# Optimization experiments

Hardware: AMD Instinct MI355X
Metric: run time of the kernel (lower is better)

Reference implementation:

```python
import jax, jax.numpy as jnp
import numpy as np
import math

B, S, HID = 1, 4096, 2048
H, KVH, D = 32, 8, 64
N_REP = H // KVH  # 4


def _rope(x, cos, sin):
    # x: [B, h, S, D]; cos/sin: [S, D//2]
    x2 = x.reshape(*x.shape[:-1], D // 2, 2)
    x0, x1 = x2[..., 0], x2[..., 1]
    c = cos[None, None, :, :]
    s = sin[None, None, :, :]
    # complex multiply (x0 + i x1) * (c + i s)
    o0 = x0 * c - x1 * s
    o1 = x0 * s + x1 * c
    return jnp.stack([o0, o1], axis=-1).reshape(x.shape)


def setup_inputs() -> dict:
    key = jax.random.key(0)
    ks = jax.random.split(key, 6)
    hidden_states = jax.random.normal(ks[0], (B, S, 2 * HID), dtype=jnp.float32)
    scale = 0.02
    wq = jax.random.normal(ks[1], (H * D, 2 * HID), dtype=jnp.float32) * scale
    wk = jax.random.normal(ks[2], (KVH * D, 2 * HID), dtype=jnp.float32) * scale
    wv = jax.random.normal(ks[3], (KVH * D, 2 * HID), dtype=jnp.float32) * scale
    wo = jax.random.normal(ks[4], (HID, H * D), dtype=jnp.float32) * scale
    # standard RoPE frequencies (theta=10000), shape [S, D//2]
    inv_freq = 1.0 / (10000.0 ** (np.arange(0, D, 2, dtype=np.float32) / D))
    angles = np.arange(S, dtype=np.float32)[:, None] * inv_freq[None, :]
    freqs_cos = jnp.asarray(np.cos(angles), dtype=jnp.float32)
    freqs_sin = jnp.asarray(np.sin(angles), dtype=jnp.float32)
    return {"hidden_states": hidden_states, "wq": wq, "wk": wk, "wv": wv,
            "wo": wo, "freqs_cos": freqs_cos, "freqs_sin": freqs_sin}


def reference(hidden_states, wq, wk, wv, wo, freqs_cos, freqs_sin):
    bsz, q_len, _ = hidden_states.shape
    q = (hidden_states @ wq.T).reshape(bsz, q_len, H, D).transpose(0, 2, 1, 3)   # [B,H,S,D]
    k = (hidden_states @ wk.T).reshape(bsz, q_len, KVH, D).transpose(0, 2, 1, 3)  # [B,KVH,S,D]
    v = (hidden_states @ wv.T).reshape(bsz, q_len, KVH, D).transpose(0, 2, 1, 3)
    q = _rope(q, freqs_cos, freqs_sin)
    k = _rope(k, freqs_cos, freqs_sin)
    # GQA repeat_kv
    k = jnp.repeat(k, N_REP, axis=1)  # [B,H,S,D]
    v = jnp.repeat(v, N_REP, axis=1)
    scores = jnp.einsum('bhqd,bhkd->bhqk', q, k) / math.sqrt(D)  # [B,H,S,S]
    weights = jax.nn.softmax(scores.astype(jnp.float32), axis=-1).astype(q.dtype)
    attn = jnp.einsum('bhqk,bhkd->bhqd', weights, v)  # [B,H,S,D]
    attn = attn.transpose(0, 2, 1, 3).reshape(bsz, q_len, H * D)
    return attn @ wo.T  # [B,S,HID]
```

## Files before the change

### kernel.cpp

```cpp
#include <hip/hip_runtime.h>
#include <hip/hip_bf16.h>

typedef __attribute__((ext_vector_type(4))) float f32x4;
typedef __attribute__((ext_vector_type(8))) __bf16 bf16x8;
typedef __attribute__((ext_vector_type(8))) short short8;
typedef __attribute__((ext_vector_type(4))) short short4v;
typedef __attribute__((ext_vector_type(2))) unsigned int uint2v;

#define SEQ 4096
#define NQKV 3072

static __device__ __forceinline__ unsigned short f2bf(float x) {
  unsigned int u = __float_as_uint(x);
  u += 0x7fffu + ((u >> 16) & 1u);
  return (unsigned short)(u >> 16);
}
static __device__ __forceinline__ float bf2f(unsigned short b) {
  return __uint_as_float(((unsigned int)b) << 16);
}
static __device__ __forceinline__ unsigned int cvtpk_bf16(float lo, float hi) {
  unsigned int r;
  asm("v_cvt_pk_bf16_f32 %0, %1, %2" : "=v"(r) : "v"(lo), "v"(hi));
  return r;
}
static __device__ __forceinline__ float exp2_fast(float x) {
  float r;
  asm("v_exp_f32 %0, %1" : "=v"(r) : "v"(x));
  return r;
}

__global__ void cvt_f32_bf16(const float* __restrict__ src,
                             unsigned short* __restrict__ dst, int n4) {
  int i = blockIdx.x * blockDim.x + threadIdx.x;
  if (i >= n4) return;
  f32x4 v = ((const f32x4*)src)[i];
  short4v o;
#pragma unroll
  for (int j = 0; j < 4; ++j) o[j] = (short)f2bf(v[j]);
  ((short4v*)dst)[i] = o;
}

template <bool OUT_F32>
__global__ __launch_bounds__(256) void gemm_bt(const unsigned short* __restrict__ A,
                                               const unsigned short* __restrict__ Bt,
                                               void* __restrict__ Cp,
                                               int M, int N, int K) {
  __shared__ unsigned short As[128 * 32];
  __shared__ unsigned short Bs[128 * 32];
  const int l = threadIdx.x & 63;
  const int wid = threadIdx.x >> 6;
  const int wr = wid >> 1, wc = wid & 1;
  const int m0 = blockIdx.y * 128, n0 = blockIdx.x * 128;
  const int lr = l & 15, lg = l >> 4;
  const int srow = l >> 2;
  const int scol = (l & 3) * 8;

  f32x4 acc[4][4];
#pragma unroll
  for (int i = 0; i < 4; ++i)
#pragma unroll
    for (int j = 0; j < 4; ++j) acc[i][j] = (f32x4){0.f, 0.f, 0.f, 0.f};

  for (int kt = 0; kt < K; kt += 32) {
#pragma unroll
    for (int i = 0; i < 2; ++i) {
      const int s = wid * 2 + i;
      const unsigned short* ga = A + (size_t)(m0 + s * 16 + srow) * K + kt + scol;
      __builtin_amdgcn_global_load_lds((const __attribute__((address_space(1))) void*)ga,
                                       (__attribute__((address_space(3))) void*)(As + s * 512),
                                       16, 0, 0);
      const unsigned short* gb = Bt + (size_t)(n0 + s * 16 + srow) * K + kt + scol;
      __builtin_amdgcn_global_load_lds((const __attribute__((address_space(1))) void*)gb,
                                       (__attribute__((address_space(3))) void*)(Bs + s * 512),
                                       16, 0, 0);
    }
    asm volatile("s_waitcnt vmcnt(0)" ::: "memory");
    __syncthreads();

    bf16x8 af[4], bfr[4];
#pragma unroll
    for (int i = 0; i < 4; ++i)
      af[i] = *(const bf16x8*)(As + (wr * 64 + i * 16 + lr) * 32 + lg * 8);
#pragma unroll
    for (int j = 0; j < 4; ++j)
      bfr[j] = *(const bf16x8*)(Bs + (wc * 64 + j * 16 + lr) * 32 + lg * 8);
#pragma unroll
    for (int i = 0; i < 4; ++i)
#pragma unroll
      for (int j = 0; j < 4; ++j)
        acc[i][j] = __builtin_amdgcn_mfma_f32_16x16x32_bf16(af[i], bfr[j], acc[i][j], 0, 0, 0);
    __syncthreads();
  }

  const int row0 = m0 + wr * 64, col0 = n0 + wc * 64;
#pragma unroll
  for (int i = 0; i < 4; ++i) {
#pragma unroll
    for (int j = 0; j < 4; ++j) {
      const int col = col0 + j * 16 + lr;
#pragma unroll
      for (int r = 0; r < 4; ++r) {
        const int row = row0 + i * 16 + lg * 4 + r;
        if (OUT_F32)
          ((float*)Cp)[(size_t)row * N + col] = acc[i][j][r];
        else
          ((unsigned short*)Cp)[(size_t)row * N + col] = f2bf(acc[i][j][r]);
      }
    }
  }
}

__global__ void rope_scale(unsigned short* __restrict__ qkv,
                           const float* __restrict__ fc,
                           const float* __restrict__ fs) {
  int idx = blockIdx.x * blockDim.x + threadIdx.x;
  int s = idx / 1280;
  int p = idx - s * 1280;
  bool isQ = (p < 1024);
  int col = isQ ? (p * 2) : (2048 + (p - 1024) * 2);
  int fi = (col >> 1) & 31;
  float c = fc[s * 32 + fi];
  float sn = fs[s * 32 + fi];
  unsigned short* ptr = qkv + (size_t)s * NQKV + col;
  float x0 = bf2f(ptr[0]);
  float x1 = bf2f(ptr[1]);
  float o0 = x0 * c - x1 * sn;
  float o1 = x0 * sn + x1 * c;
  float scl = isQ ? 0.1803368801111204f : 1.0f;
  ptr[0] = f2bf(o0 * scl);
  ptr[1] = f2bf(o1 * scl);
}

__global__ void v_transpose(const unsigned short* __restrict__ qkv,
                            unsigned short* __restrict__ Vt) {
  __shared__ unsigned short tile[64][72];
  const int kvh = blockIdx.x;
  const int st = blockIdx.y * 64;
  const int t = threadIdx.x;
  const int sl = t >> 2, d0 = (t & 3) * 16;
  const unsigned short* src = qkv + (size_t)(st + sl) * NQKV + 2560 + kvh * 64 + d0;
  *(bf16x8*)&tile[sl][d0] = *(const bf16x8*)src;
  *(bf16x8*)&tile[sl][d0 + 8] = *(const bf16x8*)(src + 8);
  __syncthreads();
  const int dl = t >> 2, s0 = (t & 3) * 16;
  unsigned short* dst = Vt + ((size_t)kvh * 64 + dl) * 4096 + st + s0;
#pragma unroll
  for (int j2 = 0; j2 < 2; ++j2) {
    short8 v;
#pragma unroll
    for (int j = 0; j < 8; ++j) v[j] = (short)tile[s0 + j2 * 8 + j][dl];
    *(short8*)(dst + j2 * 8) = v;
  }
}

__global__ __launch_bounds__(256, 4) void attn_fwd(const unsigned short* __restrict__ qkv,
                                                   const unsigned short* __restrict__ Vt,
                                                   unsigned short* __restrict__ attn) {
  __shared__ unsigned short Ks[2][4096];
  __shared__ unsigned short Vs[2][4096];
  __shared__ unsigned short Plds[4][1024];

  const int t = threadIdx.x;
  const int l = t & 63;
  const int w = t >> 6;
  const int lr = l & 15, lg = l >> 4;
  const int h = blockIdx.x;
  const int kvh = h >> 2;
  const int qbase = blockIdx.y * 128 + w * 32;

  const int chunk0 = w * 2;
  const int srow = l >> 3;
  const int scol = (l & 7) * 16;
  const int sorig = scol ^ ((srow & 7) << 4);
  const char* ksrc0 = (const char*)(qkv + 2048 + kvh * 64) +
                      (size_t)(chunk0 * 8 + srow) * (NQKV * 2) + sorig;
  const char* ksrc1 = ksrc0 + 8 * (NQKV * 2);
  const char* vsrc0 = (const char*)(Vt + (size_t)kvh * 64 * 4096) +
                      (size_t)(chunk0 * 8 + srow) * 8192 + sorig;
  const char* vsrc1 = vsrc0 + 8 * 8192;

  const int x = (lr & 7) << 4;
  const int x6 = x & 64, x45 = x & 48;
  const int offA = lr * 128 + x6 + ((lg * 16) ^ x45);
  const int offB = lr * 128 + (64 ^ x6) + ((lg * 16) ^ x45);

  const int pswz = ((lr & 7) << 4) ^ (w << 5);
  char* PldsB = (char*)Plds + w * 2048 + lr * 128;

  bf16x8 qf[2][2];
#pragma unroll
  for (int qi = 0; qi < 2; ++qi) {
    const unsigned short* qr = qkv + (size_t)(qbase + qi * 16 + lr) * NQKV + h * 64;
    qf[qi][0] = *(const bf16x8*)(qr + lg * 8);
    qf[qi][1] = *(const bf16x8*)(qr + 32 + lg * 8);
  }

  f32x4 ls4[2];
  f32x4 o[2][4];
#pragma unroll
  for (int qi = 0; qi < 2; ++qi) {
    ls4[qi] = (f32x4){0.f, 0.f, 0.f, 0.f};
#pragma unroll
    for (int c4 = 0; c4 < 4; ++c4) o[qi][c4] = (f32x4){0.f, 0.f, 0.f, 0.f};
  }

  auto stage = [&](int buf, int tile) {
    const size_t kadv = (size_t)tile * 64 * (NQKV * 2);
    const size_t vadv = (size_t)tile * 128;
    __builtin_amdgcn_global_load_lds(
        (const __attribute__((address_space(1))) void*)(ksrc0 + kadv),
        (__attribute__((address_space(3))) void*)&Ks[buf][chunk0 * 512], 16, 0, 0);
    __builtin_amdgcn_global_load_lds(
        (const __attribute__((address_space(1))) void*)(ksrc1 + kadv),
        (__attribute__((address_space(3))) void*)&Ks[buf][(chunk0 + 1) * 512], 16, 0, 0);
    __builtin_amdgcn_global_load_lds(
        (const __attribute__((address_space(1))) void*)(vsrc0 + vadv),
        (__attribute__((address_space(3))) void*)&Vs[buf][chunk0 * 512], 16, 0, 0);
    __builtin_amdgcn_global_load_lds(
        (const __attribute__((address_space(1))) void*)(vsrc1 + vadv),
        (__attribute__((address_space(3))) void*)&Vs[buf][(chunk0 + 1) * 512], 16, 0, 0);
  };

  stage(0, 0);
  asm volatile("s_waitcnt vmcnt(0)" ::: "memory");
  __syncthreads();

  const int NT = SEQ / 64;
  for (int tt = 0; tt < NT; ++tt) {
    const int buf = tt & 1;
    if (tt + 1 < NT) stage(buf ^ 1, tt + 1);

    const char* Ksb = (const char*)Ks[buf];
    const char* Vsb = (const char*)Vs[buf];

    f32x4 sc[2][4];
    __builtin_amdgcn_s_setprio(1);
#pragma unroll
    for (int sI = 0; sI < 4; ++sI) {
      bf16x8 kf0 = *(const bf16x8*)(Ksb + offA + sI * 2048);
      bf16x8 kf1 = *(const bf16x8*)(Ksb + offB + sI * 2048);
#pragma unroll
      for (int qi = 0; qi < 2; ++qi) {
        f32x4 c = (f32x4){0.f, 0.f, 0.f, 0.f};
        c = __builtin_amdgcn_mfma_f32_16x16x32_bf16(kf0, qf[qi][0], c, 0, 0, 0);
        c = __builtin_amdgcn_mfma_f32_16x16x32_bf16(kf1, qf[qi][1], c, 0, 0, 0);
        sc[qi][sI] = c;
      }
    }
    __builtin_amdgcn_s_setprio(0);

    bf16x8 pa[2][2];
#pragma unroll
    for (int qi = 0; qi < 2; ++qi) {
      float p[4][4];
#pragma unroll
      for (int sI = 0; sI < 4; ++sI)
#pragma unroll
        for (int r = 0; r < 4; ++r) p[sI][r] = exp2_fast(sc[qi][sI][r]);
#pragma unroll
      for (int sI = 0; sI < 4; ++sI)
#pragma unroll
        for (int r = 0; r < 4; ++r) ls4[qi][r] += p[sI][r];
#pragma unroll
      for (int sI = 0; sI < 4; ++sI) {
        uint2v pk;
        pk[0] = cvtpk_bf16(p[sI][0], p[sI][1]);
        pk[1] = cvtpk_bf16(p[sI][2], p[sI][3]);
        *(uint2v*)(PldsB + ((32 * sI + 8 * lg) ^ pswz)) = pk;
      }
      pa[qi][0] = *(const bf16x8*)(PldsB + ((16 * lg) ^ pswz));
      pa[qi][1] = *(const bf16x8*)(PldsB + ((64 + 16 * lg) ^ pswz));
    }

    __builtin_amdgcn_s_setprio(1);
#pragma unroll
    for (int c4 = 0; c4 < 4; ++c4) {
      bf16x8 v0 = *(const bf16x8*)(Vsb + offA + c4 * 2048);
      bf16x8 v1 = *(const bf16x8*)(Vsb + offB + c4 * 2048);
#pragma unroll
      for (int qi = 0; qi < 2; ++qi) {
        o[qi][c4] = __builtin_amdgcn_mfma_f32_16x16x32_bf16(pa[qi][0], v0, o[qi][c4], 0, 0, 0);
        o[qi][c4] = __builtin_amdgcn_mfma_f32_16x16x32_bf16(pa[qi][1], v1, o[qi][c4], 0, 0, 0);
      }
    }
    __builtin_amdgcn_s_setprio(0);

    asm volatile("s_waitcnt vmcnt(0)" ::: "memory");
    __syncthreads();
  }

#pragma unroll
  for (int qi = 0; qi < 2; ++qi) {
    float lsum = ls4[qi][0] + ls4[qi][1] + ls4[qi][2] + ls4[qi][3];
    lsum += __shfl_xor(lsum, 16, 64);
    lsum += __shfl_xor(lsum, 32, 64);
    float inv = 1.f / lsum;
    float invO[4];
#pragma unroll
    for (int r = 0; r < 4; ++r) invO[r] = __shfl(inv, 4 * lg + r, 64);
#pragma unroll
    for (int c4 = 0; c4 < 4; ++c4)
#pragma unroll
      for (int r = 0; r < 4; ++r) {
        attn[(size_t)(qbase + qi * 16 + 4 * lg + r) * 2048 + h * 64 + c4 * 16 + lr] =
            f2bf(o[qi][c4][r] * invO[r]);
      }
  }
}

extern "C" void kernel_launch(void* const* d_in, const int* in_sizes, int n_in,
                              void* d_out, int out_size, void* d_ws, size_t ws_size,
                              hipStream_t stream) {
  const float* hs = (const float*)d_in[0];
  const float* wq = (const float*)d_in[1];
  const float* wk = (const float*)d_in[2];
  const float* wv = (const float*)d_in[3];
  const float* wo = (const float*)d_in[4];
  const float* fc = (const float*)d_in[5];
  const float* fs = (const float*)d_in[6];
  float* out = (float*)d_out;

  char* ws = (char*)d_ws;
  unsigned short* Xb    = (unsigned short*)(ws);
  unsigned short* Wqkv  = (unsigned short*)(ws + (size_t)(32 << 20));
  unsigned short* Wob   = (unsigned short*)(ws + (size_t)(56 << 20));
  unsigned short* QKV   = (unsigned short*)(ws + (size_t)(64 << 20));
  unsigned short* attnb = Xb;
  unsigned short* Vtb   = (unsigned short*)(ws + (size_t)(16 << 20));

  cvt_f32_bf16<<<16384, 256, 0, stream>>>(hs, Xb, 4194304);
  cvt_f32_bf16<<<8192, 256, 0, stream>>>(wq, Wqkv, 2097152);
  cvt_f32_bf16<<<2048, 256, 0, stream>>>(wk, Wqkv + 8388608, 524288);
  cvt_f32_bf16<<<2048, 256, 0, stream>>>(wv, Wqkv + 10485760, 524288);
  cvt_f32_bf16<<<4096, 256, 0, stream>>>(wo, Wob, 1048576);

  gemm_bt<false><<<dim3(24, 32), 256, 0, stream>>>(Xb, Wqkv, QKV, 4096, 3072, 4096);

  v_transpose<<<dim3(8, 64), 256, 0, stream>>>(QKV, Vtb);
  rope_scale<<<20480, 256, 0, stream>>>(QKV, fc, fs);

  attn_fwd<<<dim3(32, 32), 256, 0, stream>>>(QKV, Vtb, attnb);

  gemm_bt<true><<<dim3(16, 32), 256, 0, stream>>>(attnb, Wob, out, 4096, 2048, 2048);
}
```

Before: 393.7 us.

## Replace GEMMs with 256-row tiles, triple-buffered LDS pipeline and swizzled loads

Both projection GEMMs are replaced by a 512-thread kernel that computes 256xBN tiles (BN=192 for QKV, 128 for the output projection). It uses three LDS buffers with prefetch two k-steps ahead, partial vmcnt waits and a single barrier per step, instead of a full drain plus two barriers each iteration. An XOR swizzle on the LDS layout reduces bank conflicts, and setprio raises wave priority around the MFMA block. The larger tiles raise MFMA work per LDS byte, at the cost of higher register and LDS pressure and fewer blocks (256 per GEMM) to fill the GPU.

```diff
diff --git a/kernel.cpp b/kernel.cpp
--- a/kernel.cpp
+++ b/kernel.cpp
@@ -40,63 +40,111 @@
   ((short4v*)dst)[i] = o;
 }
 
-template <bool OUT_F32>
-__global__ __launch_bounds__(256) void gemm_bt(const unsigned short* __restrict__ A,
-                                               const unsigned short* __restrict__ Bt,
-                                               void* __restrict__ Cp,
-                                               int M, int N, int K) {
-  __shared__ unsigned short As[128 * 32];
-  __shared__ unsigned short Bs[128 * 32];
-  const int l = threadIdx.x & 63;
-  const int wid = threadIdx.x >> 6;
-  const int wr = wid >> 1, wc = wid & 1;
-  const int m0 = blockIdx.y * 128, n0 = blockIdx.x * 128;
+template <int BN, bool OUT_F32>
+__global__ __launch_bounds__(512, 2) void gemm256(const unsigned short* __restrict__ A,
+                                                  const unsigned short* __restrict__ Bt,
+                                                  void* __restrict__ Cp,
+                                                  int M, int N, int K) {
+  constexpr int NJ = BN / 64;
+  constexpr int TC = 16 + BN / 16;
+  constexpr int SPW = (TC + 7) / 8;
+  constexpr int DUP = 8 * SPW - TC;
+
+  __shared__ unsigned short AbL[3][8192];
+  __shared__ unsigned short BbL[3][BN * 32];
+
+  const int t512 = threadIdx.x;
+  const int l = t512 & 63;
+  const int wid = t512 >> 6;
+  const int wm = wid >> 2, wn = wid & 3;
   const int lr = l & 15, lg = l >> 4;
-  const int srow = l >> 2;
-  const int scol = (l & 3) * 8;
-
-  f32x4 acc[4][4];
-#pragma unroll
-  for (int i = 0; i < 4; ++i)
-#pragma unroll
-    for (int j = 0; j < 4; ++j) acc[i][j] = (f32x4){0.f, 0.f, 0.f, 0.f};
-
-  for (int kt = 0; kt < K; kt += 32) {
-#pragma unroll
-    for (int i = 0; i < 2; ++i) {
-      const int s = wid * 2 + i;
-      const unsigned short* ga = A + (size_t)(m0 + s * 16 + srow) * K + kt + scol;
-      __builtin_amdgcn_global_load_lds((const __attribute__((address_space(1))) void*)ga,
-                                       (__attribute__((address_space(3))) void*)(As + s * 512),
-                                       16, 0, 0);
-      const unsigned short* gb = Bt + (size_t)(n0 + s * 16 + srow) * K + kt + scol;
-      __builtin_amdgcn_global_load_lds((const __attribute__((address_space(1))) void*)gb,
-                                       (__attribute__((address_space(3))) void*)(Bs + s * 512),
-                                       16, 0, 0);
-    }
-    asm volatile("s_waitcnt vmcnt(0)" ::: "memory");
-    __syncthreads();
-
-    bf16x8 af[4], bfr[4];
-#pragma unroll
-    for (int i = 0; i < 4; ++i)
-      af[i] = *(const bf16x8*)(As + (wr * 64 + i * 16 + lr) * 32 + lg * 8);
-#pragma unroll
-    for (int j = 0; j < 4; ++j)
-      bfr[j] = *(const bf16x8*)(Bs + (wc * 64 + j * 16 + lr) * 32 + lg * 8);
-#pragma unroll
-    for (int i = 0; i < 4; ++i)
-#pragma unroll
-      for (int j = 0; j < 4; ++j)
-        acc[i][j] = __builtin_amdgcn_mfma_f32_16x16x32_bf16(af[i], bfr[j], acc[i][j], 0, 0, 0);
-    __syncthreads();
-  }
-
-  const int row0 = m0 + wr * 64, col0 = n0 + wc * 64;
-#pragma unroll
-  for (int i = 0; i < 4; ++i) {
-#pragma unroll
-    for (int j = 0; j < 4; ++j) {
+  const int m0 = blockIdx.y * 256, n0 = blockIdx.x * BN;
+
+  const int lrow = l >> 2;
+  const int scb = ((l & 3) << 4) ^ ((lrow & 3) << 4);
+
+  const int rswz = (lr & 3) << 4;
+
+  f32x4 acc[8][NJ];
+#pragma unroll
+  for (int i = 0; i < 8; ++i)
+#pragma unroll
+    for (int j = 0; j < NJ; ++j) acc[i][j] = (f32x4){0.f, 0.f, 0.f, 0.f};
+
+  auto stage = [&](int buf, int t) {
+    const int kt = t * 32;
+#pragma unroll
+    for (int s = 0; s < SPW; ++s) {
+      int id = wid * SPW + s;
+      if (DUP > 0 && id >= TC) id -= DUP;
+      if (id < 16) {
+        const char* src = (const char*)(A + (size_t)(m0 + id * 16 + lrow) * K + kt) + scb;
+        __builtin_amdgcn_global_load_lds(
+            (const __attribute__((address_space(1))) void*)src,
+            (__attribute__((address_space(3))) void*)&AbL[buf][id * 512], 16, 0, 0);
+      } else {
+        const int b = id - 16;
+        const char* src = (const char*)(Bt + (size_t)(n0 + b * 16 + lrow) * K + kt) + scb;
+        __builtin_amdgcn_global_load_lds(
+            (const __attribute__((address_space(1))) void*)src,
+            (__attribute__((address_space(3))) void*)&BbL[buf][b * 512], 16, 0, 0);
+      }
+    }
+  };
+
+  const int NT = K / 32;
+
+  stage(0, 0);
+  stage(1, 1);
+  if constexpr (SPW == 4) asm volatile("s_waitcnt vmcnt(4)" ::: "memory");
+  else                    asm volatile("s_waitcnt vmcnt(3)" ::: "memory");
+  __builtin_amdgcn_s_barrier();
+  __builtin_amdgcn_sched_barrier(0);
+
+  int cur = 0;
+  for (int t = 0; t < NT; ++t) {
+    int pf = cur + 2; if (pf >= 3) pf -= 3;
+    if (t + 2 < NT) stage(pf, t + 2);
+
+    const char* Ab0 = (const char*)&AbL[cur][0] + (size_t)(wm * 128 + lr) * 64;
+    const char* Bb0 = (const char*)&BbL[cur][0] + (size_t)(wn * (BN / 4) + lr) * 64;
+    bf16x8 af[8], bfv[NJ];
+#pragma unroll
+    for (int i = 0; i < 8; ++i)
+      af[i] = *(const bf16x8*)(Ab0 + i * 1024 + ((lg * 16) ^ rswz));
+#pragma unroll
+    for (int j = 0; j < NJ; ++j)
+      bfv[j] = *(const bf16x8*)(Bb0 + j * 1024 + ((lg * 16) ^ rswz));
+
+    asm volatile("s_waitcnt lgkmcnt(0)" ::: "memory");
+    __builtin_amdgcn_sched_barrier(0);
+
+    __builtin_amdgcn_s_setprio(1);
+#pragma unroll
+    for (int i = 0; i < 8; ++i)
+#pragma unroll
+      for (int j = 0; j < NJ; ++j)
+        acc[i][j] = __builtin_amdgcn_mfma_f32_16x16x32_bf16(af[i], bfv[j], acc[i][j], 0, 0, 0);
+    __builtin_amdgcn_s_setprio(0);
+
+    if (t + 2 < NT) {
+      if constexpr (SPW == 4) asm volatile("s_waitcnt vmcnt(4)" ::: "memory");
+      else                    asm volatile("s_waitcnt vmcnt(3)" ::: "memory");
+    } else if (t + 1 < NT) {
+      asm volatile("s_waitcnt vmcnt(0)" ::: "memory");
+    }
+    if (t + 1 < NT) {
+      __builtin_amdgcn_s_barrier();
+      __builtin_amdgcn_sched_barrier(0);
+    }
+    cur = (cur == 2) ? 0 : cur + 1;
+  }
+
+  const int row0 = m0 + wm * 128, col0 = n0 + wn * (BN / 4);
+#pragma unroll
+  for (int i = 0; i < 8; ++i) {
+#pragma unroll
+    for (int j = 0; j < NJ; ++j) {
       const int col = col0 + j * 16 + lr;
 #pragma unroll
       for (int r = 0; r < 4; ++r) {
@@ -334,12 +382,12 @@
   cvt_f32_bf16<<<2048, 256, 0, stream>>>(wv, Wqkv + 10485760, 524288);
   cvt_f32_bf16<<<4096, 256, 0, stream>>>(wo, Wob, 1048576);
 
-  gemm_bt<false><<<dim3(24, 32), 256, 0, stream>>>(Xb, Wqkv, QKV, 4096, 3072, 4096);
+  gemm256<192, false><<<dim3(16, 16), 512, 0, stream>>>(Xb, Wqkv, QKV, 4096, 3072, 4096);
 
   v_transpose<<<dim3(8, 64), 256, 0, stream>>>(QKV, Vtb);
   rope_scale<<<20480, 256, 0, stream>>>(QKV, fc, fs);
 
   attn_fwd<<<dim3(32, 32), 256, 0, stream>>>(QKV, Vtb, attnb);
 
-  gemm_bt<true><<<dim3(16, 32), 256, 0, stream>>>(attnb, Wob, out, 4096, 2048, 2048);
-}
+  gemm256<128, true><<<dim3(16, 16), 512, 0, stream>>>(attnb, Wob, out, 4096, 2048, 2048);
+}
```

After: 361.1 us. 1.09x faster.
